# Kernel optimization log

Measured on AMD Instinct MI355X. Metric: run time of the kernel, lower is better.

Reference implementation:

```python
import jax, jax.numpy as jnp
import numpy as np

B, N, D, H = 1, 4096, 1024, 16
E = D // H  # head_dim = 64


def setup_inputs() -> dict:
    key = jax.random.key(0)
    ks = jax.random.split(key, 5)
    s = 0.02
    return {
        "query": jax.random.normal(ks[0], (B, N, D), dtype=jnp.float32),
        "Wq": jax.random.normal(ks[1], (D, D), dtype=jnp.float32) * s,
        "Wk": jax.random.normal(ks[2], (D, D), dtype=jnp.float32) * s,
        "Wv": jax.random.normal(ks[3], (D, D), dtype=jnp.float32) * s,
        "Wo": jax.random.normal(ks[4], (D, D), dtype=jnp.float32) * s,
        "bo": jnp.zeros((D,), dtype=jnp.float32),
    }


def reference(query, Wq, Wk, Wv, Wo, bo):
    # self-attention: key = value = query
    # nn.Linear: y = x @ W.T  (weights stored as [out, in])
    q = query @ Wq.T  # [b, n, d]
    k = query @ Wk.T
    v = query @ Wv.T
    # 'b n (h e) -> b h n e'
    q = q.reshape(B, N, H, E).transpose(0, 2, 1, 3)
    k = k.reshape(B, N, H, E).transpose(0, 2, 1, 3)
    v = v.reshape(B, N, H, E).transpose(0, 2, 1, 3)
    scale = 1.0 / jnp.sqrt(jnp.asarray(E, dtype=q.dtype))
    attn = jnp.einsum('bhne,bhme->bhnm', q, k) * scale  # [b, h, n, n]
    attn = jax.nn.softmax(attn, axis=-1)
    out = jnp.einsum('bhnm,bhme->bhne', attn, v)  # [b, h, n, e]
    # 'b h n e -> b n (h e)'
    out = out.transpose(0, 2, 1, 3).reshape(B, N, D)
    out = out @ Wo.T + bo
    return out
```

## Files before the change

kernel.cpp:

```cpp
#include <hip/hip_runtime.h>


typedef __attribute__((ext_vector_type(8))) __bf16 bf16x8;
typedef __attribute__((ext_vector_type(4))) float f32x4;
typedef __attribute__((ext_vector_type(16))) float f32x16;
typedef __attribute__((ext_vector_type(4))) unsigned short us4;
typedef __attribute__((ext_vector_type(4))) unsigned int u32x4;
typedef __attribute__((ext_vector_type(2))) unsigned int u32x2;

#define DEV __device__ __forceinline__

#define QSCALE 0.1803368801111204f

DEV unsigned short f2bf(float x) {
  union { float f; unsigned u; } c; c.f = x;
  unsigned u = c.u;
  u += 0x7FFFu + ((u >> 16) & 1u);
  return (unsigned short)(u >> 16);
}

DEV float expq(float x) {
#if __has_builtin(__builtin_amdgcn_exp2f)
  return __builtin_amdgcn_exp2f(x);
#else
  float r;
  asm("v_exp_f32 %0, %1" : "=v"(r) : "v"(x));
  return r;
#endif
}

DEV unsigned cvtpk_bf16(float lo, float hi) {
  unsigned r;
  asm("v_cvt_pk_bf16_f32 %0, %1, %2" : "=v"(r) : "v"(lo), "v"(hi));
  return r;
}

DEV void plswap_u(unsigned& a, unsigned& b) {
#if __has_builtin(__builtin_amdgcn_permlane32_swap)
  u32x2 r = __builtin_amdgcn_permlane32_swap(a, b, false, false);
  a = r.x; b = r.y;
#else
  asm("v_permlane32_swap_b32 %0, %1" : "+v"(a), "+v"(b));
#endif
}

DEV void plswap_f(float& a, float& b) {
  unsigned ua = __float_as_uint(a), ub = __float_as_uint(b);
  plswap_u(ua, ub);
  a = __uint_as_float(ua); b = __uint_as_float(ub);
}

DEV void gload16(const void* g, void* lds) {
  __builtin_amdgcn_global_load_lds(
      (const __attribute__((address_space(1))) unsigned int*)g,
      (__attribute__((address_space(3))) unsigned int*)lds, 16, 0, 0);
}

__global__ void cast_bf16_kernel(const float* __restrict__ in,
                                 unsigned short* __restrict__ out, int n4) {
  int i = blockIdx.x * 256 + threadIdx.x;
  if (i >= n4) return;
  float4 v = reinterpret_cast<const float4*>(in)[i];
  us4 o;
  o.x = f2bf(v.x); o.y = f2bf(v.y); o.z = f2bf(v.z); o.w = f2bf(v.w);
  reinterpret_cast<us4*>(out)[i] = o;
}

__global__ void cast4_bf16_kernel(const float* __restrict__ a,
                                  const float* __restrict__ b,
                                  const float* __restrict__ c,
                                  const float* __restrict__ d,
                                  unsigned short* __restrict__ out, int n4) {
  const int y = blockIdx.y;
  const float* src = y == 0 ? a : (y == 1 ? b : (y == 2 ? c : d));
  int i = blockIdx.x * 256 + threadIdx.x;
  if (i >= n4) return;
  float4 v = reinterpret_cast<const float4*>(src)[i];
  us4 o;
  o.x = f2bf(v.x); o.y = f2bf(v.y); o.z = f2bf(v.z); o.w = f2bf(v.w);
  reinterpret_cast<us4*>(out + (size_t)y * n4 * 4)[i] = o;
}

__global__ void transpose_v(const unsigned short* __restrict__ V,
                            unsigned short* __restrict__ Vt) {
  __shared__ unsigned short tile[64][65];
  const int t = threadIdx.x;
  const int bc = blockIdx.x * 64;
  const int br = blockIdx.y * 64;
#pragma unroll
  for (int i = 0; i < 16; ++i) {
    int idx = i * 256 + t;
    int r = idx >> 6, c = idx & 63;
    tile[r][c] = V[(size_t)(br + r) * 1024 + bc + c];
  }
  __syncthreads();
#pragma unroll
  for (int i = 0; i < 16; ++i) {
    int idx = i * 256 + t;
    int r = idx >> 6, c = idx & 63;
    Vt[(size_t)(bc + r) * 4096 + br + c] = tile[c][r];
  }
}

__global__ __launch_bounds__(256)
void gemm_qkv(const unsigned short* __restrict__ A,
              const unsigned short* __restrict__ B,
              unsigned short* __restrict__ Qo,
              unsigned short* __restrict__ Ko,
              unsigned short* __restrict__ Vo) {
  constexpr int K = 1024, BK = 64;
  __shared__ unsigned short As[128 * BK];
  __shared__ unsigned short Bs[128 * BK];
  const int t = threadIdx.x;
  const int w = t >> 6, l = t & 63;
  const int brow = blockIdx.x * 128;
  const int bcol = blockIdx.y * 128;
  const int wr = w >> 1, wc = w & 1;
  const int lr = l >> 3;
  const int lc = ((l & 7) ^ lr) * 8;
  const int fr = l & 15;
  const int fcb = (l >> 4) * 16;
  const int swz = (l & 7) << 4;

  f32x4 acc[4][4] = {};
  const char* Asb = (const char*)As;
  const char* Bsb = (const char*)Bs;

  for (int k0 = 0; k0 < K; k0 += BK) {
#pragma unroll
    for (int i = 0; i < 4; ++i) {
      const int r = w * 32 + i * 8;
      gload16(A + (size_t)(brow + r + lr) * K + k0 + lc, (void*)(As + r * BK));
      gload16(B + (size_t)(bcol + r + lr) * K + k0 + lc, (void*)(Bs + r * BK));
    }
    __syncthreads();
#pragma unroll
    for (int kk = 0; kk < 2; ++kk) {
      bf16x8 af[4], bfr[4];
#pragma unroll
      for (int m = 0; m < 4; ++m)
        af[m] = *(const bf16x8*)(Asb + (wr * 64 + m * 16 + fr) * 128 +
                                 ((kk * 64 + fcb) ^ swz));
#pragma unroll
      for (int n = 0; n < 4; ++n)
        bfr[n] = *(const bf16x8*)(Bsb + (wc * 64 + n * 16 + fr) * 128 +
                                  ((kk * 64 + fcb) ^ swz));
#pragma unroll
      for (int m = 0; m < 4; ++m)
#pragma unroll
        for (int n = 0; n < 4; ++n)
          acc[m][n] = __builtin_amdgcn_mfma_f32_16x16x32_bf16(
              af[m], bfr[n], acc[m][n], 0, 0, 0);
    }
    __syncthreads();
  }

  const int seg = blockIdx.y >> 3;
  unsigned short* dst = seg == 0 ? Qo : (seg == 1 ? Ko : Vo);
  const float sc = seg == 0 ? QSCALE : 1.0f;
  const int orow = brow + wr * 64 + (l >> 4) * 4;
  const int ocol = (blockIdx.y & 7) * 128 + wc * 64 + fr;
#pragma unroll
  for (int m = 0; m < 4; ++m)
#pragma unroll
    for (int n = 0; n < 4; ++n)
#pragma unroll
      for (int j = 0; j < 4; ++j)
        dst[(size_t)(orow + m * 16 + j) * 1024 + (ocol + n * 16)] =
            f2bf(acc[m][n][j] * sc);
}

__global__ __launch_bounds__(256)
void gemm_out64(const unsigned short* __restrict__ A,
                const unsigned short* __restrict__ B,
                float* __restrict__ C, const float* __restrict__ bias) {
  constexpr int N = 1024, K = 1024, BK = 64;
  __shared__ unsigned short As[64 * BK];
  __shared__ unsigned short Bs[128 * BK];
  const int t = threadIdx.x;
  const int w = t >> 6, l = t & 63;
  const int brow = blockIdx.x * 64;
  const int bcol = blockIdx.y * 128;
  const int wr = w >> 1, wc = w & 1;
  const int lr = l >> 3;
  const int lc = ((l & 7) ^ lr) * 8;
  const int fr = l & 15;
  const int fcb = (l >> 4) * 16;
  const int swz = (l & 7) << 4;

  f32x4 acc[2][4] = {};
  const char* Asb = (const char*)As;
  const char* Bsb = (const char*)Bs;

  for (int k0 = 0; k0 < K; k0 += BK) {
#pragma unroll
    for (int i = 0; i < 2; ++i) {
      const int r = w * 16 + i * 8;
      gload16(A + (size_t)(brow + r + lr) * K + k0 + lc, (void*)(As + r * BK));
    }
#pragma unroll
    for (int i = 0; i < 4; ++i) {
      const int r = w * 32 + i * 8;
      gload16(B + (size_t)(bcol + r + lr) * K + k0 + lc, (void*)(Bs + r * BK));
    }
    __syncthreads();
#pragma unroll
    for (int kk = 0; kk < 2; ++kk) {
      bf16x8 af[2], bfr[4];
#pragma unroll
      for (int m = 0; m < 2; ++m)
        af[m] = *(const bf16x8*)(Asb + (wr * 32 + m * 16 + fr) * 128 +
                                 ((kk * 64 + fcb) ^ swz));
#pragma unroll
      for (int n = 0; n < 4; ++n)
        bfr[n] = *(const bf16x8*)(Bsb + (wc * 64 + n * 16 + fr) * 128 +
                                  ((kk * 64 + fcb) ^ swz));
#pragma unroll
      for (int m = 0; m < 2; ++m)
#pragma unroll
        for (int n = 0; n < 4; ++n)
          acc[m][n] = __builtin_amdgcn_mfma_f32_16x16x32_bf16(
              af[m], bfr[n], acc[m][n], 0, 0, 0);
    }
    __syncthreads();
  }

  const int orow = brow + wr * 32 + (l >> 4) * 4;
  const int ocol = bcol + wc * 64 + fr;
#pragma unroll
  for (int m = 0; m < 2; ++m)
#pragma unroll
    for (int n = 0; n < 4; ++n)
#pragma unroll
      for (int j = 0; j < 4; ++j)
        C[(size_t)(orow + m * 16 + j) * N + (ocol + n * 16)] =
            acc[m][n][j] + bias[ocol + n * 16];
}

__global__ __launch_bounds__(512, 4)
void attn_v6(const unsigned short* __restrict__ Q,
             const unsigned short* __restrict__ Km,
             const unsigned short* __restrict__ Vt,
             unsigned short* __restrict__ AO) {
  constexpr int N = 4096, D = 1024, KB = 64, NT = N / KB;
  __shared__ unsigned long long LDSA[65536 / 8];
  char* LDS = (char*)LDSA;
  const int t = threadIdx.x, w = t >> 6, l = t & 63;
  const int g = w >> 2, wg = w & 3;
  const int flat = blockIdx.x;
  const int c = flat & 7, ii = flat >> 3;
  const int h = c * 2 + (ii >> 5);
  const int qt = ii & 31;
  const int q0 = qt * 128 + wg * 32;
  const int ln = l & 31, hi = l >> 5;
  const int lr = l >> 3;
  const int lc8 = ((l & 7) ^ lr) * 8;
  const int swz = (l & 7) << 4;

  char* kb0 = LDS + (g * 2 + 0) * 8192;
  char* kb1 = LDS + (g * 2 + 1) * 8192;
  char* vb0 = LDS + 32768 + (g * 2 + 0) * 8192;
  char* vb1 = LDS + 32768 + (g * 2 + 1) * 8192;

  bf16x8 qf[4];
  {
    const unsigned short* qp = Q + (size_t)(q0 + ln) * D + h * 64 + hi * 8;
#pragma unroll
    for (int ks = 0; ks < 4; ++ks) qf[ks] = *(const bf16x8*)(qp + ks * 16);
  }

  f32x16 oacc0 = {}, oacc1 = {};
  float lsum = 0.f;

  auto stage = [&](char* kd, char* vd, int kv0) {
#pragma unroll
    for (int s = 0; s < 2; ++s) {
      const int r0 = wg * 16 + s * 8;
      gload16(Km + (size_t)(kv0 + r0 + lr) * D + h * 64 + lc8,
              (void*)(kd + r0 * 128));
      gload16(Vt + (size_t)(h * 64 + r0 + lr) * N + kv0 + lc8,
              (void*)(vd + r0 * 128));
    }
  };

  stage(kb0, vb0, g * KB);
  __syncthreads();

  for (int i = 0; i < NT / 2; ++i) {
    const char* ksb = (i & 1) ? kb1 : kb0;
    const char* vsb = (i & 1) ? vb1 : vb0;
    if (i + 1 < NT / 2)
      stage((i & 1) ? kb0 : kb1, (i & 1) ? vb0 : vb1, (2 * (i + 1) + g) * KB);

    f32x16 sa = {}, sb = {};
    __builtin_amdgcn_s_setprio(1);
#pragma unroll
    for (int ks = 0; ks < 4; ++ks) {
      bf16x8 kf0 = *(const bf16x8*)(ksb + (0 * 32 + ln) * 128 +
                                    ((ks * 32 + hi * 16) ^ swz));
      bf16x8 kf1 = *(const bf16x8*)(ksb + (1 * 32 + ln) * 128 +
                                    ((ks * 32 + hi * 16) ^ swz));
      sa = __builtin_amdgcn_mfma_f32_32x32x16_bf16(kf0, qf[ks], sa, 0, 0, 0);
      sb = __builtin_amdgcn_mfma_f32_32x32x16_bf16(kf1, qf[ks], sb, 0, 0, 0);
    }
    __builtin_amdgcn_s_setprio(0);

#pragma unroll
    for (int r = 0; r < 16; ++r) { sa[r] = expq(sa[r]); sb[r] = expq(sb[r]); }
    {
      float red[16];
#pragma unroll
      for (int r = 0; r < 16; ++r) red[r] = sa[r] + sb[r];
#pragma unroll
      for (int s = 8; s >= 1; s >>= 1)
#pragma unroll
        for (int r = 0; r < s; ++r) red[r] += red[r + s];
      lsum += red[0];
    }

    unsigned pw[4][4];
#pragma unroll
    for (int kvs = 0; kvs < 4; ++kvs) {
      const f32x16& S = (kvs < 2) ? sa : sb;
      const int rb = (kvs & 1) * 8;
      unsigned A0 = cvtpk_bf16(S[rb + 0], S[rb + 1]);
      unsigned B0 = cvtpk_bf16(S[rb + 4], S[rb + 5]);
      unsigned A1 = cvtpk_bf16(S[rb + 2], S[rb + 3]);
      unsigned B1 = cvtpk_bf16(S[rb + 6], S[rb + 7]);
      plswap_u(A0, B0);
      plswap_u(A1, B1);
      pw[kvs][0] = A0; pw[kvs][1] = A1; pw[kvs][2] = B0; pw[kvs][3] = B1;
    }

    __builtin_amdgcn_s_setprio(1);
#pragma unroll
    for (int kvs = 0; kvs < 4; ++kvs) {
      u32x4 pv = {pw[kvs][0], pw[kvs][1], pw[kvs][2], pw[kvs][3]};
      bf16x8 pf = __builtin_bit_cast(bf16x8, pv);
      bf16x8 vf0 = *(const bf16x8*)(vsb + (0 * 32 + ln) * 128 +
                                    ((kvs * 32 + hi * 16) ^ swz));
      bf16x8 vf1 = *(const bf16x8*)(vsb + (1 * 32 + ln) * 128 +
                                    ((kvs * 32 + hi * 16) ^ swz));
      oacc0 = __builtin_amdgcn_mfma_f32_32x32x16_bf16(vf0, pf, oacc0, 0, 0, 0);
      oacc1 = __builtin_amdgcn_mfma_f32_32x32x16_bf16(vf1, pf, oacc1, 0, 0, 0);
    }
    __builtin_amdgcn_s_setprio(0);

    __syncthreads();
  }

  float* cb = (float*)LDS;
  float* cl = (float*)(LDS + 32768);
  if (g == 1) {
    float* p = cb + (wg * 64 + l) * 32;
#pragma unroll
    for (int r = 0; r < 16; ++r) { p[r] = oacc0[r]; p[16 + r] = oacc1[r]; }
    cl[wg * 64 + l] = lsum;
  }
  __syncthreads();
  if (g == 0) {
    float* p = cb + (wg * 64 + l) * 32;
#pragma unroll
    for (int r = 0; r < 16; ++r) { oacc0[r] += p[r]; oacc1[r] += p[16 + r]; }
    lsum += cl[wg * 64 + l];
    float sa2 = lsum, sb2 = lsum;
    plswap_f(sa2, sb2);
    const float inv = 1.0f / (sa2 + sb2);

    char* Osc = LDS + 34816 + wg * 4096;
#pragma unroll
    for (int es = 0; es < 2; ++es)
#pragma unroll
      for (int gg = 0; gg < 4; ++gg)
#pragma unroll
        for (int c2 = 0; c2 < 2; ++c2) {
          const f32x16& oa = es == 0 ? oacc0 : oacc1;
          unsigned pk = cvtpk_bf16(oa[gg * 4 + c2 * 2] * inv,
                                   oa[gg * 4 + c2 * 2 + 1] * inv);
          const int col = es * 64 + gg * 16 + hi * 8 + c2 * 4;
          *(unsigned*)(Osc + ln * 128 + (col ^ ((ln & 7) << 4))) = pk;
        }
#pragma unroll
    for (int p2 = 0; p2 < 4; ++p2) {
      const int q = p2 * 8 + lr;
      bf16x8 ov = *(const bf16x8*)(Osc + q * 128 + (((l & 7) ^ lr) << 4));
      *(bf16x8*)(AO + (size_t)(q0 + q) * D + h * 64 + (l & 7) * 8) = ov;
    }
  }
}

extern "C" void kernel_launch(void* const* d_in, const int* in_sizes, int n_in,
                              void* d_out, int out_size, void* d_ws, size_t ws_size,
                              hipStream_t stream) {
  const float* query = (const float*)d_in[0];
  const float* Wq    = (const float*)d_in[1];
  const float* Wk    = (const float*)d_in[2];
  const float* Wv    = (const float*)d_in[3];
  const float* Wo    = (const float*)d_in[4];
  const float* bo    = (const float*)d_in[5];
  float* out = (float*)d_out;

  char* ws = (char*)d_ws;
  const size_t MB = 1024 * 1024;
  unsigned short* Wqkv_b = (unsigned short*)(ws + 0 * MB);
  unsigned short* Wo_b   = (unsigned short*)(ws + 6 * MB);
  unsigned short* Xb     = (unsigned short*)(ws + 8 * MB);
  unsigned short* Qb     = (unsigned short*)(ws + 16 * MB);
  unsigned short* Kb     = (unsigned short*)(ws + 24 * MB);
  unsigned short* Vb     = (unsigned short*)(ws + 32 * MB);
  unsigned short* Vtb    = (unsigned short*)(ws + 40 * MB);
  unsigned short* AOb    = (unsigned short*)(ws + 32 * MB);

  {
    int n4 = (4096 * 1024) / 4;
    cast_bf16_kernel<<<dim3((n4 + 255) / 256), dim3(256), 0, stream>>>(query, Xb, n4);
    n4 = (1024 * 1024) / 4;
    cast4_bf16_kernel<<<dim3((n4 + 255) / 256, 4), dim3(256), 0, stream>>>(
        Wq, Wk, Wv, Wo, Wqkv_b, n4);
  }

  gemm_qkv<<<dim3(32, 24), dim3(256), 0, stream>>>(Xb, Wqkv_b, Qb, Kb, Vb);

  transpose_v<<<dim3(16, 64), dim3(256), 0, stream>>>(Vb, Vtb);

  attn_v6<<<dim3(512), dim3(512), 0, stream>>>(Qb, Kb, Vtb, AOb);

  gemm_out64<<<dim3(64, 8), dim3(256), 0, stream>>>(AOb, Wo_b, out, bo);
}
```

Baseline: 152.8 us.

## Process 64 query rows per wave in attention to reuse K/V fragments

Halves the attention block to 256 threads (4 waves). Each wave now handles two 32-row query tiles, so every K and V fragment read from LDS feeds two MFMAs instead of one. This cuts LDS read traffic per FLOP and halves the number of waves doing redundant fragment loads. In exchange it roughly doubles accumulator register use per wave, lowers the occupancy bound, and gives each wave more staging loads to issue.

```diff
diff --git a/kernel.cpp b/kernel.cpp
--- a/kernel.cpp
+++ b/kernel.cpp
@@ -237,8 +237,8 @@
             acc[m][n][j] + bias[ocol + n * 16];
 }
 
-__global__ __launch_bounds__(512, 4)
-void attn_v6(const unsigned short* __restrict__ Q,
+__global__ __launch_bounds__(256, 2)
+void attn_v7(const unsigned short* __restrict__ Q,
              const unsigned short* __restrict__ Km,
              const unsigned short* __restrict__ Vt,
              unsigned short* __restrict__ AO) {
@@ -246,12 +246,12 @@
   __shared__ unsigned long long LDSA[65536 / 8];
   char* LDS = (char*)LDSA;
   const int t = threadIdx.x, w = t >> 6, l = t & 63;
-  const int g = w >> 2, wg = w & 3;
+  const int g = w >> 1, wq = w & 1;
   const int flat = blockIdx.x;
   const int c = flat & 7, ii = flat >> 3;
   const int h = c * 2 + (ii >> 5);
   const int qt = ii & 31;
-  const int q0 = qt * 128 + wg * 32;
+  const int q0 = qt * 128 + wq * 64;
   const int ln = l & 31, hi = l >> 5;
   const int lr = l >> 3;
   const int lc8 = ((l & 7) ^ lr) * 8;
@@ -262,20 +262,24 @@
   char* vb0 = LDS + 32768 + (g * 2 + 0) * 8192;
   char* vb1 = LDS + 32768 + (g * 2 + 1) * 8192;
 
-  bf16x8 qf[4];
+  bf16x8 qfA[4], qfB[4];
   {
-    const unsigned short* qp = Q + (size_t)(q0 + ln) * D + h * 64 + hi * 8;
-#pragma unroll
-    for (int ks = 0; ks < 4; ++ks) qf[ks] = *(const bf16x8*)(qp + ks * 16);
-  }
-
-  f32x16 oacc0 = {}, oacc1 = {};
-  float lsum = 0.f;
+    const unsigned short* qa = Q + (size_t)(q0 + ln) * D + h * 64 + hi * 8;
+    const unsigned short* qb = Q + (size_t)(q0 + 32 + ln) * D + h * 64 + hi * 8;
+#pragma unroll
+    for (int ks = 0; ks < 4; ++ks) {
+      qfA[ks] = *(const bf16x8*)(qa + ks * 16);
+      qfB[ks] = *(const bf16x8*)(qb + ks * 16);
+    }
+  }
+
+  f32x16 oA0 = {}, oA1 = {}, oB0 = {}, oB1 = {};
+  float lsumA = 0.f, lsumB = 0.f;
 
   auto stage = [&](char* kd, char* vd, int kv0) {
 #pragma unroll
-    for (int s = 0; s < 2; ++s) {
-      const int r0 = wg * 16 + s * 8;
+    for (int s = 0; s < 4; ++s) {
+      const int r0 = wq * 32 + s * 8;
       gload16(Km + (size_t)(kv0 + r0 + lr) * D + h * 64 + lc8,
               (void*)(kd + r0 * 128));
       gload16(Vt + (size_t)(h * 64 + r0 + lr) * N + kv0 + lc8,
@@ -292,7 +296,7 @@
     if (i + 1 < NT / 2)
       stage((i & 1) ? kb0 : kb1, (i & 1) ? vb0 : vb1, (2 * (i + 1) + g) * KB);
 
-    f32x16 sa = {}, sb = {};
+    f32x16 sA0 = {}, sA1 = {}, sB0 = {}, sB1 = {};
     __builtin_amdgcn_s_setprio(1);
 #pragma unroll
     for (int ks = 0; ks < 4; ++ks) {
@@ -300,49 +304,77 @@
                                     ((ks * 32 + hi * 16) ^ swz));
       bf16x8 kf1 = *(const bf16x8*)(ksb + (1 * 32 + ln) * 128 +
                                     ((ks * 32 + hi * 16) ^ swz));
-      sa = __builtin_amdgcn_mfma_f32_32x32x16_bf16(kf0, qf[ks], sa, 0, 0, 0);
-      sb = __builtin_amdgcn_mfma_f32_32x32x16_bf16(kf1, qf[ks], sb, 0, 0, 0);
+      sA0 = __builtin_amdgcn_mfma_f32_32x32x16_bf16(kf0, qfA[ks], sA0, 0, 0, 0);
+      sA1 = __builtin_amdgcn_mfma_f32_32x32x16_bf16(kf1, qfA[ks], sA1, 0, 0, 0);
+      sB0 = __builtin_amdgcn_mfma_f32_32x32x16_bf16(kf0, qfB[ks], sB0, 0, 0, 0);
+      sB1 = __builtin_amdgcn_mfma_f32_32x32x16_bf16(kf1, qfB[ks], sB1, 0, 0, 0);
     }
     __builtin_amdgcn_s_setprio(0);
 
 #pragma unroll
-    for (int r = 0; r < 16; ++r) { sa[r] = expq(sa[r]); sb[r] = expq(sb[r]); }
+    for (int r = 0; r < 16; ++r) {
+      sA0[r] = expq(sA0[r]); sA1[r] = expq(sA1[r]);
+      sB0[r] = expq(sB0[r]); sB1[r] = expq(sB1[r]);
+    }
     {
       float red[16];
 #pragma unroll
-      for (int r = 0; r < 16; ++r) red[r] = sa[r] + sb[r];
+      for (int r = 0; r < 16; ++r) red[r] = sA0[r] + sA1[r];
 #pragma unroll
       for (int s = 8; s >= 1; s >>= 1)
 #pragma unroll
         for (int r = 0; r < s; ++r) red[r] += red[r + s];
-      lsum += red[0];
-    }
-
-    unsigned pw[4][4];
+      lsumA += red[0];
+#pragma unroll
+      for (int r = 0; r < 16; ++r) red[r] = sB0[r] + sB1[r];
+#pragma unroll
+      for (int s = 8; s >= 1; s >>= 1)
+#pragma unroll
+        for (int r = 0; r < s; ++r) red[r] += red[r + s];
+      lsumB += red[0];
+    }
+
+    unsigned pwA[4][4], pwB[4][4];
 #pragma unroll
     for (int kvs = 0; kvs < 4; ++kvs) {
-      const f32x16& S = (kvs < 2) ? sa : sb;
       const int rb = (kvs & 1) * 8;
-      unsigned A0 = cvtpk_bf16(S[rb + 0], S[rb + 1]);
-      unsigned B0 = cvtpk_bf16(S[rb + 4], S[rb + 5]);
-      unsigned A1 = cvtpk_bf16(S[rb + 2], S[rb + 3]);
-      unsigned B1 = cvtpk_bf16(S[rb + 6], S[rb + 7]);
-      plswap_u(A0, B0);
-      plswap_u(A1, B1);
-      pw[kvs][0] = A0; pw[kvs][1] = A1; pw[kvs][2] = B0; pw[kvs][3] = B1;
+      {
+        const f32x16& S = (kvs < 2) ? sA0 : sA1;
+        unsigned A0 = cvtpk_bf16(S[rb + 0], S[rb + 1]);
+        unsigned B0 = cvtpk_bf16(S[rb + 4], S[rb + 5]);
+        unsigned A1 = cvtpk_bf16(S[rb + 2], S[rb + 3]);
+        unsigned B1 = cvtpk_bf16(S[rb + 6], S[rb + 7]);
+        plswap_u(A0, B0);
+        plswap_u(A1, B1);
+        pwA[kvs][0] = A0; pwA[kvs][1] = A1; pwA[kvs][2] = B0; pwA[kvs][3] = B1;
+      }
+      {
+        const f32x16& S = (kvs < 2) ? sB0 : sB1;
+        unsigned A0 = cvtpk_bf16(S[rb + 0], S[rb + 1]);
+        unsigned B0 = cvtpk_bf16(S[rb + 4], S[rb + 5]);
+        unsigned A1 = cvtpk_bf16(S[rb + 2], S[rb + 3]);
+        unsigned B1 = cvtpk_bf16(S[rb + 6], S[rb + 7]);
+        plswap_u(A0, B0);
+        plswap_u(A1, B1);
+        pwB[kvs][0] = A0; pwB[kvs][1] = A1; pwB[kvs][2] = B0; pwB[kvs][3] = B1;
+      }
     }
 
     __builtin_amdgcn_s_setprio(1);
 #pragma unroll
     for (int kvs = 0; kvs < 4; ++kvs) {
-      u32x4 pv = {pw[kvs][0], pw[kvs][1], pw[kvs][2], pw[kvs][3]};
-      bf16x8 pf = __builtin_bit_cast(bf16x8, pv);
+      u32x4 pva = {pwA[kvs][0], pwA[kvs][1], pwA[kvs][2], pwA[kvs][3]};
+      u32x4 pvb = {pwB[kvs][0], pwB[kvs][1], pwB[kvs][2], pwB[kvs][3]};
+      bf16x8 pfA = __builtin_bit_cast(bf16x8, pva);
+      bf16x8 pfB = __builtin_bit_cast(bf16x8, pvb);
       bf16x8 vf0 = *(const bf16x8*)(vsb + (0 * 32 + ln) * 128 +
                                     ((kvs * 32 + hi * 16) ^ swz));
       bf16x8 vf1 = *(const bf16x8*)(vsb + (1 * 32 + ln) * 128 +
                                     ((kvs * 32 + hi * 16) ^ swz));
-      oacc0 = __builtin_amdgcn_mfma_f32_32x32x16_bf16(vf0, pf, oacc0, 0, 0, 0);
-      oacc1 = __builtin_amdgcn_mfma_f32_32x32x16_bf16(vf1, pf, oacc1, 0, 0, 0);
+      oA0 = __builtin_amdgcn_mfma_f32_32x32x16_bf16(vf0, pfA, oA0, 0, 0, 0);
+      oA1 = __builtin_amdgcn_mfma_f32_32x32x16_bf16(vf1, pfA, oA1, 0, 0, 0);
+      oB0 = __builtin_amdgcn_mfma_f32_32x32x16_bf16(vf0, pfB, oB0, 0, 0, 0);
+      oB1 = __builtin_amdgcn_mfma_f32_32x32x16_bf16(vf1, pfB, oB1, 0, 0, 0);
     }
     __builtin_amdgcn_s_setprio(0);
 
@@ -352,36 +384,53 @@
   float* cb = (float*)LDS;
   float* cl = (float*)(LDS + 32768);
   if (g == 1) {
-    float* p = cb + (wg * 64 + l) * 32;
-#pragma unroll
-    for (int r = 0; r < 16; ++r) { p[r] = oacc0[r]; p[16 + r] = oacc1[r]; }
-    cl[wg * 64 + l] = lsum;
+    float* pa = cb + ((wq * 2 + 0) * 64 + l) * 32;
+    float* pb = cb + ((wq * 2 + 1) * 64 + l) * 32;
+#pragma unroll
+    for (int r = 0; r < 16; ++r) {
+      pa[r] = oA0[r]; pa[16 + r] = oA1[r];
+      pb[r] = oB0[r]; pb[16 + r] = oB1[r];
+    }
+    cl[(wq * 2 + 0) * 64 + l] = lsumA;
+    cl[(wq * 2 + 1) * 64 + l] = lsumB;
   }
   __syncthreads();
   if (g == 0) {
-    float* p = cb + (wg * 64 + l) * 32;
-#pragma unroll
-    for (int r = 0; r < 16; ++r) { oacc0[r] += p[r]; oacc1[r] += p[16 + r]; }
-    lsum += cl[wg * 64 + l];
-    float sa2 = lsum, sb2 = lsum;
+    float* pa = cb + ((wq * 2 + 0) * 64 + l) * 32;
+    float* pb = cb + ((wq * 2 + 1) * 64 + l) * 32;
+#pragma unroll
+    for (int r = 0; r < 16; ++r) {
+      oA0[r] += pa[r]; oA1[r] += pa[16 + r];
+      oB0[r] += pb[r]; oB1[r] += pb[16 + r];
+    }
+    lsumA += cl[(wq * 2 + 0) * 64 + l];
+    lsumB += cl[(wq * 2 + 1) * 64 + l];
+    float sa2 = lsumA, sb2 = lsumA;
     plswap_f(sa2, sb2);
-    const float inv = 1.0f / (sa2 + sb2);
-
-    char* Osc = LDS + 34816 + wg * 4096;
+    const float invA = 1.0f / (sa2 + sb2);
+    float sa3 = lsumB, sb3 = lsumB;
+    plswap_f(sa3, sb3);
+    const float invB = 1.0f / (sa3 + sb3);
+
+    char* Osc = LDS + 33792 + wq * 8192;
 #pragma unroll
     for (int es = 0; es < 2; ++es)
 #pragma unroll
       for (int gg = 0; gg < 4; ++gg)
 #pragma unroll
         for (int c2 = 0; c2 < 2; ++c2) {
-          const f32x16& oa = es == 0 ? oacc0 : oacc1;
-          unsigned pk = cvtpk_bf16(oa[gg * 4 + c2 * 2] * inv,
-                                   oa[gg * 4 + c2 * 2 + 1] * inv);
           const int col = es * 64 + gg * 16 + hi * 8 + c2 * 4;
+          const f32x16& oa = es == 0 ? oA0 : oA1;
+          unsigned pk = cvtpk_bf16(oa[gg * 4 + c2 * 2] * invA,
+                                   oa[gg * 4 + c2 * 2 + 1] * invA);
           *(unsigned*)(Osc + ln * 128 + (col ^ ((ln & 7) << 4))) = pk;
+          const f32x16& ob = es == 0 ? oB0 : oB1;
+          unsigned pk2 = cvtpk_bf16(ob[gg * 4 + c2 * 2] * invB,
+                                    ob[gg * 4 + c2 * 2 + 1] * invB);
+          *(unsigned*)(Osc + (32 + ln) * 128 + (col ^ ((ln & 7) << 4))) = pk2;
         }
 #pragma unroll
-    for (int p2 = 0; p2 < 4; ++p2) {
+    for (int p2 = 0; p2 < 8; ++p2) {
       const int q = p2 * 8 + lr;
       bf16x8 ov = *(const bf16x8*)(Osc + q * 128 + (((l & 7) ^ lr) << 4));
       *(bf16x8*)(AO + (size_t)(q0 + q) * D + h * 64 + (l & 7) * 8) = ov;
@@ -423,7 +472,7 @@
 
   transpose_v<<<dim3(16, 64), dim3(256), 0, stream>>>(Vb, Vtb);
 
-  attn_v6<<<dim3(512), dim3(512), 0, stream>>>(Qb, Kb, Vtb, AOb);
+  attn_v7<<<dim3(512), dim3(256), 0, stream>>>(Qb, Kb, Vtb, AOb);
 
   gemm_out64<<<dim3(64, 8), dim3(256), 0, stream>>>(AOb, Wo_b, out, bo);
 }
```

Measured after the change: 154.6 us. No clear change (+1.2%).

## Pre-pack K and V into MFMA fragment-ordered tiles for contiguous attention loads

Applied to the files above, without the earlier changes.

The QKV GEMM now writes K straight into a per-head, per-64-row tile layout ordered to match the MFMA fragment layout. The V transpose kernel is replaced by a repack into the same tiled layout. The attention kernel then stages each K/V tile as one contiguous 8 KB block and reads fragments with simple linear LDS offsets, with no XOR swizzle. This is meant to make global loads fully coalesced and cut address math, but it drops the swizzle, which may add LDS bank conflicts, and the K epilogue now does scattered 2-byte stores.

```diff
diff --git a/kernel.cpp b/kernel.cpp
--- a/kernel.cpp
+++ b/kernel.cpp
@@ -81,8 +81,8 @@
   reinterpret_cast<us4*>(out + (size_t)y * n4 * 4)[i] = o;
 }
 
-__global__ void transpose_v(const unsigned short* __restrict__ V,
-                            unsigned short* __restrict__ Vt) {
+__global__ void repack_v(const unsigned short* __restrict__ V,
+                         unsigned short* __restrict__ Vp) {
   __shared__ unsigned short tile[64][65];
   const int t = threadIdx.x;
   const int bc = blockIdx.x * 64;
@@ -94,11 +94,12 @@
     tile[r][c] = V[(size_t)(br + r) * 1024 + bc + c];
   }
   __syncthreads();
+  const int obase = ((bc >> 6) * 64 + (br >> 6)) * 4096;
 #pragma unroll
   for (int i = 0; i < 16; ++i) {
-    int idx = i * 256 + t;
-    int r = idx >> 6, c = idx & 63;
-    Vt[(size_t)(bc + r) * 4096 + br + c] = tile[c][r];
+    int id = i * 256 + t;
+    int f = id >> 9, rem = id & 511, e = rem >> 3, kv8 = rem & 7;
+    Vp[obase + id] = tile[f * 8 + kv8][e];
   }
 }
 
@@ -156,18 +157,33 @@
   }
 
   const int seg = blockIdx.y >> 3;
-  unsigned short* dst = seg == 0 ? Qo : (seg == 1 ? Ko : Vo);
-  const float sc = seg == 0 ? QSCALE : 1.0f;
   const int orow = brow + wr * 64 + (l >> 4) * 4;
   const int ocol = (blockIdx.y & 7) * 128 + wc * 64 + fr;
-#pragma unroll
-  for (int m = 0; m < 4; ++m)
-#pragma unroll
-    for (int n = 0; n < 4; ++n)
-#pragma unroll
-      for (int j = 0; j < 4; ++j)
-        dst[(size_t)(orow + m * 16 + j) * 1024 + (ocol + n * 16)] =
-            f2bf(acc[m][n][j] * sc);
+  if (seg == 1) {
+#pragma unroll
+    for (int n = 0; n < 4; ++n) {
+      const int col = ocol + n * 16;
+      const int bn = (col >> 6) * 262144 + ((col & 63) >> 3) * 512 + (col & 7);
+#pragma unroll
+      for (int m = 0; m < 4; ++m)
+#pragma unroll
+        for (int j = 0; j < 4; ++j) {
+          const int row = orow + m * 16 + j;
+          Ko[bn + (row >> 6) * 4096 + (row & 63) * 8] = f2bf(acc[m][n][j]);
+        }
+    }
+  } else {
+    unsigned short* dst = seg == 0 ? Qo : Vo;
+    const float sc = seg == 0 ? QSCALE : 1.0f;
+#pragma unroll
+    for (int m = 0; m < 4; ++m)
+#pragma unroll
+      for (int n = 0; n < 4; ++n)
+#pragma unroll
+        for (int j = 0; j < 4; ++j)
+          dst[(size_t)(orow + m * 16 + j) * 1024 + (ocol + n * 16)] =
+              f2bf(acc[m][n][j] * sc);
+  }
 }
 
 __global__ __launch_bounds__(256)
@@ -238,11 +254,11 @@
 }
 
 __global__ __launch_bounds__(512, 4)
-void attn_v6(const unsigned short* __restrict__ Q,
-             const unsigned short* __restrict__ Km,
-             const unsigned short* __restrict__ Vt,
+void attn_v8(const unsigned short* __restrict__ Q,
+             const unsigned short* __restrict__ Kp,
+             const unsigned short* __restrict__ Vp,
              unsigned short* __restrict__ AO) {
-  constexpr int N = 4096, D = 1024, KB = 64, NT = N / KB;
+  constexpr int N = 4096, D = 1024, NT = N / 64;
   __shared__ unsigned long long LDSA[65536 / 8];
   char* LDS = (char*)LDSA;
   const int t = threadIdx.x, w = t >> 6, l = t & 63;
@@ -254,8 +270,7 @@
   const int q0 = qt * 128 + wg * 32;
   const int ln = l & 31, hi = l >> 5;
   const int lr = l >> 3;
-  const int lc8 = ((l & 7) ^ lr) * 8;
-  const int swz = (l & 7) << 4;
+  const int ko = hi * 1024 + ln * 16;
 
   char* kb0 = LDS + (g * 2 + 0) * 8192;
   char* kb1 = LDS + (g * 2 + 1) * 8192;
@@ -272,34 +287,35 @@
   f32x16 oacc0 = {}, oacc1 = {};
   float lsum = 0.f;
 
-  auto stage = [&](char* kd, char* vd, int kv0) {
+  const char* Kp8 = (const char*)Kp;
+  const char* Vp8 = (const char*)Vp;
+
+  auto stage = [&](char* kd, char* vd, int kvt) {
+    const char* Kt = Kp8 + (size_t)(h * 64 + kvt) * 8192;
+    const char* Vt = Vp8 + (size_t)(h * 64 + kvt) * 8192;
 #pragma unroll
     for (int s = 0; s < 2; ++s) {
-      const int r0 = wg * 16 + s * 8;
-      gload16(Km + (size_t)(kv0 + r0 + lr) * D + h * 64 + lc8,
-              (void*)(kd + r0 * 128));
-      gload16(Vt + (size_t)(h * 64 + r0 + lr) * N + kv0 + lc8,
-              (void*)(vd + r0 * 128));
+      const int off = (wg * 2 + s) * 1024;
+      gload16(Kt + off + l * 16, (void*)(kd + off));
+      gload16(Vt + off + l * 16, (void*)(vd + off));
     }
   };
 
-  stage(kb0, vb0, g * KB);
+  stage(kb0, vb0, g);
   __syncthreads();
 
   for (int i = 0; i < NT / 2; ++i) {
     const char* ksb = (i & 1) ? kb1 : kb0;
     const char* vsb = (i & 1) ? vb1 : vb0;
     if (i + 1 < NT / 2)
-      stage((i & 1) ? kb0 : kb1, (i & 1) ? vb0 : vb1, (2 * (i + 1) + g) * KB);
+      stage((i & 1) ? kb0 : kb1, (i & 1) ? vb0 : vb1, 2 * (i + 1) + g);
 
     f32x16 sa = {}, sb = {};
     __builtin_amdgcn_s_setprio(1);
 #pragma unroll
     for (int ks = 0; ks < 4; ++ks) {
-      bf16x8 kf0 = *(const bf16x8*)(ksb + (0 * 32 + ln) * 128 +
-                                    ((ks * 32 + hi * 16) ^ swz));
-      bf16x8 kf1 = *(const bf16x8*)(ksb + (1 * 32 + ln) * 128 +
-                                    ((ks * 32 + hi * 16) ^ swz));
+      bf16x8 kf0 = *(const bf16x8*)(ksb + ks * 2048 + ko);
+      bf16x8 kf1 = *(const bf16x8*)(ksb + ks * 2048 + 512 + ko);
       sa = __builtin_amdgcn_mfma_f32_32x32x16_bf16(kf0, qf[ks], sa, 0, 0, 0);
       sb = __builtin_amdgcn_mfma_f32_32x32x16_bf16(kf1, qf[ks], sb, 0, 0, 0);
     }
@@ -337,10 +353,8 @@
     for (int kvs = 0; kvs < 4; ++kvs) {
       u32x4 pv = {pw[kvs][0], pw[kvs][1], pw[kvs][2], pw[kvs][3]};
       bf16x8 pf = __builtin_bit_cast(bf16x8, pv);
-      bf16x8 vf0 = *(const bf16x8*)(vsb + (0 * 32 + ln) * 128 +
-                                    ((kvs * 32 + hi * 16) ^ swz));
-      bf16x8 vf1 = *(const bf16x8*)(vsb + (1 * 32 + ln) * 128 +
-                                    ((kvs * 32 + hi * 16) ^ swz));
+      bf16x8 vf0 = *(const bf16x8*)(vsb + kvs * 2048 + ko);
+      bf16x8 vf1 = *(const bf16x8*)(vsb + kvs * 2048 + 512 + ko);
       oacc0 = __builtin_amdgcn_mfma_f32_32x32x16_bf16(vf0, pf, oacc0, 0, 0, 0);
       oacc1 = __builtin_amdgcn_mfma_f32_32x32x16_bf16(vf1, pf, oacc1, 0, 0, 0);
     }
@@ -421,9 +435,9 @@
 
   gemm_qkv<<<dim3(32, 24), dim3(256), 0, stream>>>(Xb, Wqkv_b, Qb, Kb, Vb);
 
-  transpose_v<<<dim3(16, 64), dim3(256), 0, stream>>>(Vb, Vtb);
-
-  attn_v6<<<dim3(512), dim3(512), 0, stream>>>(Qb, Kb, Vtb, AOb);
+  repack_v<<<dim3(16, 64), dim3(256), 0, stream>>>(Vb, Vtb);
+
+  attn_v8<<<dim3(512), dim3(512), 0, stream>>>(Qb, Kb, Vtb, AOb);
 
   gemm_out64<<<dim3(64, 8), dim3(256), 0, stream>>>(AOb, Wo_b, out, bo);
 }
```

Result: no change. 151.5 us (-0.9%).
